# Kernel optimization log

Measured on AMD Instinct MI355X. Metric: run time of the kernel, lower is better.

The kernel has to match this reference:

```python
import jax, jax.numpy as jnp
import numpy as np

B, T, D, H = 4, 2048, 1024, 16
DEPTH = D // H
MASK_NEG = 1e10


def setup_inputs() -> dict:
    key = jax.random.key(0)
    k1, k2, k3 = jax.random.split(key, 3)
    x = jax.random.normal(k1, (B, T, D), dtype=jnp.float32)
    w_attn = jax.random.normal(k2, (D, 3 * D), dtype=jnp.float32) * 0.02
    b_attn = jnp.zeros((3 * D,), dtype=jnp.float32)
    w_proj = jax.random.normal(k3, (D, D), dtype=jnp.float32) * 0.02
    b_proj = jnp.zeros((D,), dtype=jnp.float32)
    return {"x": x, "w_attn": w_attn, "b_attn": b_attn,
            "w_proj": w_proj, "b_proj": b_proj}


def _split_heads(t):
    # (B, T, D) -> (B, H, T, depth)
    return t.reshape(B, T, H, DEPTH).transpose(0, 2, 1, 3)


def reference(x, w_attn, b_attn, w_proj, b_proj):
    # fused QKV projection (GPT-2 conv1d == dense)
    qkv = x @ w_attn + b_attn                      # (B, T, 3D)
    q, k, v = jnp.split(qkv, 3, axis=2)
    q, k, v = _split_heads(q), _split_heads(k), _split_heads(v)
    present = jnp.stack([k, v], axis=1)            # (B, 2, H, T, depth)

    # scaled scores with additive causal mask (as in source: w*b - 1e10*(1-b))
    scores = jnp.einsum('bhqd,bhkd->bhqk', q, k) / jnp.sqrt(
        jnp.asarray(DEPTH, dtype=x.dtype))
    i = jnp.arange(T)[:, None]
    j = jnp.arange(T)[None, :]
    b = (i >= j).astype(scores.dtype)              # (T, T) lower-tri incl diag
    scores = scores * b - MASK_NEG * (1.0 - b)
    attn = jax.nn.softmax(scores, axis=-1)         # (B, H, T, T)

    out = jnp.einsum('bhqk,bhkd->bhqd', attn, v)   # (B, H, T, depth)
    out = out.transpose(0, 2, 1, 3).reshape(B, T, D)
    out = out @ w_proj + b_proj                    # (B, T, D)
    return out, present
```

## Files before the change

### kernel.cpp

```cpp
#include <hip/hip_runtime.h>
#include <hip/hip_bf16.h>
#include <cstdint>
#include <cstddef>

typedef __bf16 y8 __attribute__((ext_vector_type(8)));
typedef float f4 __attribute__((ext_vector_type(4)));
typedef unsigned short u16t;

#define NB 4
#define TT 2048
#define DD 1024
#define HH 16

static constexpr size_t OUT0 = (size_t)NB * TT * DD;
#define QSCALE 0.180336880111120426f

__device__ __forceinline__ u16t bf16r(float f) {
    union { float f; unsigned u; } x; x.f = f;
    return (u16t)((x.u + 0x7FFFu + ((x.u >> 16) & 1u)) >> 16);
}

__device__ __forceinline__ unsigned cvtpk(float lo, float hi) {
    unsigned r;
    asm("v_cvt_pk_bf16_f32 %0, %1, %2" : "=v"(r) : "v"(lo), "v"(hi));
    return r;
}

#define GLDS16(g, s) __builtin_amdgcn_global_load_lds( \
    (__attribute__((address_space(1))) void*)(g),      \
    (__attribute__((address_space(3))) void*)(s), 16, 0, 0)

#define BARX() asm volatile("s_barrier" ::: "memory")
#define VMW(n) asm volatile("s_waitcnt vmcnt(" #n ")" ::: "memory")
#define LGKM0() asm volatile("s_waitcnt lgkmcnt(0)" ::: "memory")

__global__ __launch_bounds__(256)
void cvt_f32_bf16(const float* __restrict__ in, u16t* __restrict__ outp, int n) {
    int i = (blockIdx.x * 256 + threadIdx.x) * 8;
    if (i >= n) return;
    float4 a = *(const float4*)(in + i);
    float4 b = *(const float4*)(in + i + 4);
    union { u16t h[8]; uint4 q; } u;
    u.h[0] = bf16r(a.x); u.h[1] = bf16r(a.y); u.h[2] = bf16r(a.z); u.h[3] = bf16r(a.w);
    u.h[4] = bf16r(b.x); u.h[5] = bf16r(b.y); u.h[6] = bf16r(b.z); u.h[7] = bf16r(b.w);
    *(uint4*)(outp + i) = u.q;
}

__global__ __launch_bounds__(256)
void transpose_w(const float* __restrict__ in, u16t* __restrict__ outp, int Kd, int Nd,
                 int qlim, float qs) {
    __shared__ float tile[32][33];
    const int n0 = blockIdx.x * 32, k0 = blockIdx.y * 32;
    const int tx = threadIdx.x & 31, ty = threadIdx.x >> 5;
    for (int yy = ty; yy < 32; yy += 8)
        tile[yy][tx] = in[(size_t)(k0 + yy) * Nd + n0 + tx];
    __syncthreads();
    for (int yy = ty; yy < 32; yy += 8) {
        float v = tile[tx][yy];
        if (n0 + yy < qlim) v *= qs;
        outp[(size_t)(n0 + yy) * Kd + k0 + tx] = bf16r(v);
    }
}

template<int MODE>
__global__ __launch_bounds__(512, 1)
void gemm_bt(const u16t* __restrict__ A, const u16t* __restrict__ Bt,
             const float* __restrict__ bias, float* __restrict__ C,
             float* __restrict__ pres, u16t* __restrict__ qb,
             u16t* __restrict__ kb, u16t* __restrict__ vtb,
             int N, int K)
{
    __shared__ char sm[98304];
    char* const smA0 = sm;
    char* const smB0 = sm + 65536;
    const int tid = threadIdx.x;
    const int w = tid >> 6, l = tid & 63;
    const int wr = w >> 1, wc = w & 1;
    const int lr = l & 15, lq = l >> 4;
    const int idx = blockIdx.x;
    const int bm = (idx & 31) << 8;
    const int bn = (idx >> 5) << 7;

    auto stage = [&](int k0, int pi) {
#pragma unroll
        for (int c = 0; c < 4; ++c) {
            const int L = (tid << 4) + (c << 13);
            const int row = L >> 7;
            const int col = (((L >> 4) & 7) ^ (row & 7)) << 3;
            GLDS16(A + (size_t)(bm + row) * K + k0 + col,
                   smA0 + (pi << 15) + L);
        }
#pragma unroll
        for (int c = 0; c < 2; ++c) {
            const int L = (tid << 4) + (c << 13);
            const int row = L >> 7;
            const int col = (((L >> 4) & 7) ^ (row & 7)) << 3;
            GLDS16(Bt + (size_t)(bn + row) * K + k0 + col,
                   smB0 + (pi << 14) + L);
        }
    };

    f4 acc[4][4] = {};
    const int nt = K >> 6;

    stage(0, 0);
    for (int t = 0; t < nt; ++t) {
        if (t + 1 < nt) { stage((t + 1) << 6, (t + 1) & 1); VMW(6); }
        else            { VMW(0); }
        BARX();
        const char* La = smA0 + ((t & 1) << 15);
        const char* Lb = smB0 + ((t & 1) << 14);
#pragma unroll
        for (int ks = 0; ks < 2; ++ks) {
            y8 af[4], bfv[4];
#pragma unroll
            for (int m = 0; m < 4; ++m) {
                const int row = wr * 64 + m * 16 + lr;
                const int slot = (lq + ks * 4) ^ (row & 7);
                af[m] = *(const y8*)(La + row * 128 + (slot << 4));
            }
#pragma unroll
            for (int n = 0; n < 4; ++n) {
                const int row = wc * 64 + n * 16 + lr;
                const int slot = (lq + ks * 4) ^ (row & 7);
                bfv[n] = *(const y8*)(Lb + row * 128 + (slot << 4));
            }
#pragma unroll
            for (int m = 0; m < 4; ++m)
#pragma unroll
                for (int n = 0; n < 4; ++n)
                    acc[m][n] = __builtin_amdgcn_mfma_f32_16x16x32_bf16(af[m], bfv[n], acc[m][n], 0, 0, 0);
        }
        BARX();
    }

    if (MODE == 0) {
#pragma unroll
        for (int m = 0; m < 4; ++m) {
            const int rowb = bm + wr * 64 + m * 16 + 4 * lq;
#pragma unroll
            for (int n = 0; n < 4; ++n) {
                const int col = bn + wc * 64 + n * 16 + lr;
                const float bv = bias[col];
#pragma unroll
                for (int r = 0; r < 4; ++r)
                    C[(size_t)(rowb + r) * N + col] = acc[m][n][r] + bv;
            }
        }
    } else {
        const int part = bn >> 10;

        if (part == 2) {
#pragma unroll
            for (int m = 0; m < 4; ++m) {
                const int rowb = bm + wr * 64 + m * 16 + 4 * lq;
                const int b0 = rowb >> 11, t0 = rowb & 2047;
#pragma unroll
                for (int n = 0; n < 4; ++n) {
                    const int colg = bn + wc * 64 + n * 16 + lr;
                    const float bv = bias[colg];
                    const int cl = colg & 1023;
                    const int h = cl >> 6, d = cl & 63;
                    uint2 pk;
                    pk.x = cvtpk(acc[m][n][0] + bv, acc[m][n][1] + bv);
                    pk.y = cvtpk(acc[m][n][2] + bv, acc[m][n][3] + bv);
                    *(uint2*)(vtb + ((size_t)(b0 * HH + h) * 64 + d) * TT + t0) = pk;
                }
            }
        }

#pragma unroll
        for (int m = 0; m < 4; ++m)
#pragma unroll
            for (int n = 0; n < 4; ++n) {
                const int co = wc * 64 + n * 16 + lr;
                float bv = bias[bn + co];
                if (part == 0) bv *= QSCALE;
#pragma unroll
                for (int r = 0; r < 4; ++r) {
                    const int ro = wr * 64 + m * 16 + 4 * lq + r;
                    *(u16t*)(smA0 + ro * 256 + (((co >> 3) ^ (ro & 7)) << 4)
                             + ((co & 7) << 1)) = bf16r(acc[m][n][r] + bv);
                }
            }
        LGKM0();
        BARX();

        const int hb = (bn & 1023) >> 6;
        const int c = tid & 15;
        const int rw = tid >> 4;
        const int h2 = hb + (c >> 3);
        const int d0 = (c & 7) * 8;
#pragma unroll
        for (int s = 0; s < 8; ++s) {
            const int row = s * 32 + rw;
            union { y8 v; uint4 q; u16t h[8]; } u;
            u.v = *(const y8*)(smA0 + row * 256 + ((c ^ (row & 7)) << 4));
            const int tglob = bm + row;
            const int b0 = tglob >> 11, tt = tglob & 2047;
            const size_t base = (((size_t)(b0 * HH + h2)) * TT + tt) * 64 + d0;
            if (part == 0) {
                *(uint4*)(qb + base) = u.q;
            } else {
                if (part == 1) *(uint4*)(kb + base) = u.q;
                float4 f0, f1;
                f0.x = __uint_as_float((unsigned)u.h[0] << 16);
                f0.y = __uint_as_float((unsigned)u.h[1] << 16);
                f0.z = __uint_as_float((unsigned)u.h[2] << 16);
                f0.w = __uint_as_float((unsigned)u.h[3] << 16);
                f1.x = __uint_as_float((unsigned)u.h[4] << 16);
                f1.y = __uint_as_float((unsigned)u.h[5] << 16);
                f1.z = __uint_as_float((unsigned)u.h[6] << 16);
                f1.w = __uint_as_float((unsigned)u.h[7] << 16);
                const size_t pb = OUT0 +
                    (((size_t)((b0 * 2 + (part - 1)) * HH + h2)) * TT + tt) * 64 + d0;
                *(float4*)(pres + pb) = f0;
                *(float4*)(pres + pb + 4) = f1;
            }
        }
    }
}

__global__ __launch_bounds__(256, 3)
void attn_fwd(const u16t* __restrict__ qg, const u16t* __restrict__ kg,
              const u16t* __restrict__ vtg, u16t* __restrict__ og)
{
    __shared__ u16t sQP[128 * 64];
    __shared__ u16t sK[2 * 64 * 64];
    __shared__ u16t sV[2 * 64 * 64];
    const int tid = threadIdx.x;
    const int w = tid >> 6, l = tid & 63;
    const int lr = l & 15, lq = l >> 4;
    const int qt = 15 - blockIdx.y;
    const int bh = blockIdx.x;
    const int b = bh >> 4, h = bh & 15;
    const u16t* qsrc = qg + (size_t)bh * TT * 64;
    const u16t* ksrc = kg + (size_t)bh * TT * 64;
    const u16t* vsrc = vtg + (size_t)bh * 64 * TT;

    auto stageKV = [&](int kt, int pi) {
        const int kv0 = kt << 6;
#pragma unroll
        for (int c = 0; c < 2; ++c) {
            const int L = ((w * 64 + l) << 4) + (c << 12);
            const int row = L >> 7;
            const int col = (((L >> 4) & 7) ^ (row & 7)) << 3;
            GLDS16(ksrc + (kv0 + row) * 64 + col,
                   (char*)sK + (pi << 13) + (w << 10) + (c << 12));
            GLDS16(vsrc + (size_t)row * TT + kv0 + col,
                   (char*)sV + (pi << 13) + (w << 10) + (c << 12));
        }
    };

#pragma unroll
    for (int c = 0; c < 4; ++c) {
        const int L = ((w * 64 + l) << 4) + (c << 12);
        const int row = L >> 7;
        const int col = (((L >> 4) & 7) ^ (row & 7)) << 3;
        GLDS16(qsrc + (qt * 128 + row) * 64 + col, (char*)sQP + (w << 10) + (c << 12));
    }
    stageKV(0, 0);
    __syncthreads();

    y8 qf[2][2];
#pragma unroll
    for (int qm = 0; qm < 2; ++qm)
#pragma unroll
        for (int ks = 0; ks < 2; ++ks) {
            const int row = w * 32 + qm * 16 + lr;
            const int slot = (lq + ks * 4) ^ (row & 7);
            qf[qm][ks] = *(const y8*)((const char*)sQP + row * 128 + (slot << 4));
        }

    f4 o[2][4] = {};
    float lsum[2] = {0.f, 0.f};

    char* Pw = (char*)sQP + (w << 12);
    const int qmax = qt * 128 + w * 32 + 31;
    const int ktiles = 2 * qt + 2;
    int cur = 0;

    for (int kt = 0; kt < ktiles; ++kt) {
        __syncthreads();
        if (kt + 1 < ktiles) stageKV(kt + 1, cur ^ 1);
        const int kv0 = kt << 6;
        if (kv0 <= qmax) {
            const char* Kb = (const char*)sK + (cur << 13);
            const char* Vb = (const char*)sV + (cur << 13);

            f4 s[2][4] = {};
            __builtin_amdgcn_s_setprio(1);
#pragma unroll
            for (int ks = 0; ks < 2; ++ks) {
                y8 kf[4];
#pragma unroll
                for (int n = 0; n < 4; ++n) {
                    const int row = n * 16 + lr;
                    const int slot = (lq + ks * 4) ^ (row & 7);
                    kf[n] = *(const y8*)(Kb + row * 128 + (slot << 4));
                }
#pragma unroll
                for (int qm = 0; qm < 2; ++qm)
#pragma unroll
                    for (int n = 0; n < 4; ++n)
                        s[qm][n] = __builtin_amdgcn_mfma_f32_16x16x32_bf16(kf[n], qf[qm][ks], s[qm][n], 0, 0, 0);
            }
            __builtin_amdgcn_s_setprio(0);

#pragma unroll
            for (int qm = 0; qm < 2; ++qm) {
                const int qb0 = qt * 128 + w * 32 + qm * 16;
                if (kv0 + 63 > qb0) {
                    const int query = qb0 + lr;
#pragma unroll
                    for (int n = 0; n < 4; ++n)
#pragma unroll
                        for (int r = 0; r < 4; ++r)
                            if (kv0 + n * 16 + 4 * lq + r > query) s[qm][n][r] = -1e30f;
                }

                float rs = 0.f;
#pragma unroll
                for (int n = 0; n < 4; ++n)
#pragma unroll
                    for (int r = 0; r < 4; ++r) {
                        const float p = exp2f(s[qm][n][r]);
                        s[qm][n][r] = p;
                        rs += p;
                    }
                lsum[qm] += rs;

                const int prow = qm * 16 + lr;
                const int rbase = prow * 128 + ((lq & 1) << 3);
#pragma unroll
                for (int n = 0; n < 4; ++n) {
                    uint2 pk;
                    pk.x = cvtpk(s[qm][n][0], s[qm][n][1]);
                    pk.y = cvtpk(s[qm][n][2], s[qm][n][3]);
                    const int sIdx = 2 * n + (lq >> 1);
                    *(uint2*)(Pw + rbase + ((sIdx ^ (prow & 7)) << 4)) = pk;
                }
            }

            __builtin_amdgcn_s_setprio(1);
#pragma unroll
            for (int ks = 0; ks < 2; ++ks) {
                y8 vf[4], pf[2];
#pragma unroll
                for (int n = 0; n < 4; ++n) {
                    const int row = n * 16 + lr;
                    const int slot = (lq + ks * 4) ^ (row & 7);
                    vf[n] = *(const y8*)(Vb + row * 128 + (slot << 4));
                }
#pragma unroll
                for (int qm = 0; qm < 2; ++qm) {
                    const int row = qm * 16 + lr;
                    const int slot = (lq + ks * 4) ^ (row & 7);
                    pf[qm] = *(const y8*)(Pw + row * 128 + (slot << 4));
                }
#pragma unroll
                for (int qm = 0; qm < 2; ++qm)
#pragma unroll
                    for (int n = 0; n < 4; ++n)
                        o[qm][n] = __builtin_amdgcn_mfma_f32_16x16x32_bf16(vf[n], pf[qm], o[qm][n], 0, 0, 0);
            }
            __builtin_amdgcn_s_setprio(0);
        }
        cur ^= 1;
    }

#pragma unroll
    for (int qm = 0; qm < 2; ++qm) {
        float t = lsum[qm];
        t += __shfl_xor(t, 16);
        t += __shfl_xor(t, 32);
        const float inv = 1.0f / t;
        const int trow = qt * 128 + w * 32 + qm * 16 + lr;
#pragma unroll
        for (int n = 0; n < 4; ++n) {
            uint2 pk;
            pk.x = cvtpk(o[qm][n][0] * inv, o[qm][n][1] * inv);
            pk.y = cvtpk(o[qm][n][2] * inv, o[qm][n][3] * inv);
            *(uint2*)(og + ((size_t)(b * TT + trow)) * DD + h * 64 + n * 16 + 4 * lq) = pk;
        }
    }
}

extern "C" void kernel_launch(void* const* d_in, const int* in_sizes, int n_in,
                              void* d_out, int out_size, void* d_ws, size_t ws_size,
                              hipStream_t stream) {
    const float* x      = (const float*)d_in[0];
    const float* w_attn = (const float*)d_in[1];
    const float* b_attn = (const float*)d_in[2];
    const float* w_proj = (const float*)d_in[3];
    const float* b_proj = (const float*)d_in[4];
    float* outp = (float*)d_out;
    char* ws = (char*)d_ws;

    u16t* xb  = (u16t*)(ws + 0);
    u16t* wta = (u16t*)(ws + 16777216);
    u16t* wtp = (u16t*)(ws + 23068672);
    u16t* qb  = (u16t*)(ws + 25165824);
    u16t* kb  = (u16t*)(ws + 41943040);
    u16t* vtb = (u16t*)(ws + 58720256);
    if (ws_size < 75497472) return;

    cvt_f32_bf16<<<4096, 256, 0, stream>>>(x, xb, 8388608);
    transpose_w<<<dim3(96, 32), 256, 0, stream>>>(w_attn, wta, 1024, 3072, 1024, QSCALE);
    transpose_w<<<dim3(32, 32), 256, 0, stream>>>(w_proj, wtp, 1024, 1024, 0, 1.0f);

    gemm_bt<1><<<768, 512, 0, stream>>>(xb, wta, b_attn, nullptr, outp,
                                        qb, kb, vtb, 3072, 1024);
    attn_fwd<<<dim3(64, 16), 256, 0, stream>>>(qb, kb, vtb, xb );
    gemm_bt<0><<<256, 512, 0, stream>>>(xb, wtp, b_proj, outp,
                                        nullptr, nullptr, nullptr, nullptr,
                                        1024, 1024);
}
```

Before: 179.0 us.

## Fuse prep kernels into one launch and double attention query tile to 256

Merges the three preprocessing kernels (x conversion and two weight transposes) into one launch with a block-index switch, removing two launch gaps. The attention kernel now uses 512 threads (8 waves) per block, covering 256 query rows instead of 128. Each staged K/V tile is therefore reused by twice as many waves, halving K/V traffic per query. The trade-off is half as many blocks (512), coarser causal load balance, and more LDS per block.

```diff
diff --git a/kernel.cpp b/kernel.cpp
--- a/kernel.cpp
+++ b/kernel.cpp
@@ -35,22 +35,32 @@
 #define LGKM0() asm volatile("s_waitcnt lgkmcnt(0)" ::: "memory")
 
 __global__ __launch_bounds__(256)
-void cvt_f32_bf16(const float* __restrict__ in, u16t* __restrict__ outp, int n) {
-    int i = (blockIdx.x * 256 + threadIdx.x) * 8;
-    if (i >= n) return;
-    float4 a = *(const float4*)(in + i);
-    float4 b = *(const float4*)(in + i + 4);
-    union { u16t h[8]; uint4 q; } u;
-    u.h[0] = bf16r(a.x); u.h[1] = bf16r(a.y); u.h[2] = bf16r(a.z); u.h[3] = bf16r(a.w);
-    u.h[4] = bf16r(b.x); u.h[5] = bf16r(b.y); u.h[6] = bf16r(b.z); u.h[7] = bf16r(b.w);
-    *(uint4*)(outp + i) = u.q;
-}
-
-__global__ __launch_bounds__(256)
-void transpose_w(const float* __restrict__ in, u16t* __restrict__ outp, int Kd, int Nd,
-                 int qlim, float qs) {
+void prep(const float* __restrict__ x, u16t* __restrict__ xb,
+          const float* __restrict__ w_attn, u16t* __restrict__ wta,
+          const float* __restrict__ w_proj, u16t* __restrict__ wtp)
+{
+    const int bid = blockIdx.x;
+    if (bid < 4096) {
+        const int i = (bid * 256 + threadIdx.x) * 8;
+        float4 a = *(const float4*)(x + i);
+        float4 b = *(const float4*)(x + i + 4);
+        union { u16t h[8]; uint4 q; } u;
+        u.h[0] = bf16r(a.x); u.h[1] = bf16r(a.y); u.h[2] = bf16r(a.z); u.h[3] = bf16r(a.w);
+        u.h[4] = bf16r(b.x); u.h[5] = bf16r(b.y); u.h[6] = bf16r(b.z); u.h[7] = bf16r(b.w);
+        *(uint4*)(xb + i) = u.q;
+        return;
+    }
     __shared__ float tile[32][33];
-    const int n0 = blockIdx.x * 32, k0 = blockIdx.y * 32;
+    const float* in; u16t* outp; int Nd, n0, k0, qlim; float qs;
+    if (bid < 7168) {
+        const int j = bid - 4096;
+        in = w_attn; outp = wta; Nd = 3072;
+        n0 = (j % 96) * 32; k0 = (j / 96) * 32; qlim = 1024; qs = QSCALE;
+    } else {
+        const int j = bid - 7168;
+        in = w_proj; outp = wtp; Nd = 1024;
+        n0 = (j & 31) * 32; k0 = (j >> 5) * 32; qlim = 0; qs = 1.0f;
+    }
     const int tx = threadIdx.x & 31, ty = threadIdx.x >> 5;
     for (int yy = ty; yy < 32; yy += 8)
         tile[yy][tx] = in[(size_t)(k0 + yy) * Nd + n0 + tx];
@@ -58,7 +68,7 @@
     for (int yy = ty; yy < 32; yy += 8) {
         float v = tile[tx][yy];
         if (n0 + yy < qlim) v *= qs;
-        outp[(size_t)(n0 + yy) * Kd + k0 + tx] = bf16r(v);
+        outp[(size_t)(n0 + yy) * 1024 + k0 + tx] = bf16r(v);
     }
 }
 
@@ -221,17 +231,17 @@
     }
 }
 
-__global__ __launch_bounds__(256, 3)
+__global__ __launch_bounds__(512, 4)
 void attn_fwd(const u16t* __restrict__ qg, const u16t* __restrict__ kg,
               const u16t* __restrict__ vtg, u16t* __restrict__ og)
 {
-    __shared__ u16t sQP[128 * 64];
+    __shared__ u16t sQP[256 * 64];
     __shared__ u16t sK[2 * 64 * 64];
     __shared__ u16t sV[2 * 64 * 64];
     const int tid = threadIdx.x;
     const int w = tid >> 6, l = tid & 63;
     const int lr = l & 15, lq = l >> 4;
-    const int qt = 15 - blockIdx.y;
+    const int qt = 7 - blockIdx.y;
     const int bh = blockIdx.x;
     const int b = bh >> 4, h = bh & 15;
     const u16t* qsrc = qg + (size_t)bh * TT * 64;
@@ -240,24 +250,19 @@
 
     auto stageKV = [&](int kt, int pi) {
         const int kv0 = kt << 6;
-#pragma unroll
-        for (int c = 0; c < 2; ++c) {
-            const int L = ((w * 64 + l) << 4) + (c << 12);
-            const int row = L >> 7;
-            const int col = (((L >> 4) & 7) ^ (row & 7)) << 3;
-            GLDS16(ksrc + (kv0 + row) * 64 + col,
-                   (char*)sK + (pi << 13) + (w << 10) + (c << 12));
-            GLDS16(vsrc + (size_t)row * TT + kv0 + col,
-                   (char*)sV + (pi << 13) + (w << 10) + (c << 12));
-        }
-    };
-
-#pragma unroll
-    for (int c = 0; c < 4; ++c) {
-        const int L = ((w * 64 + l) << 4) + (c << 12);
+        const int L = tid << 4;
         const int row = L >> 7;
         const int col = (((L >> 4) & 7) ^ (row & 7)) << 3;
-        GLDS16(qsrc + (qt * 128 + row) * 64 + col, (char*)sQP + (w << 10) + (c << 12));
+        GLDS16(ksrc + (kv0 + row) * 64 + col, (char*)sK + (pi << 13) + L);
+        GLDS16(vsrc + (size_t)row * TT + kv0 + col, (char*)sV + (pi << 13) + L);
+    };
+
+#pragma unroll
+    for (int c = 0; c < 4; ++c) {
+        const int L = (tid << 4) + (c << 13);
+        const int row = L >> 7;
+        const int col = (((L >> 4) & 7) ^ (row & 7)) << 3;
+        GLDS16(qsrc + (qt * 256 + row) * 64 + col, (char*)sQP + L);
     }
     stageKV(0, 0);
     __syncthreads();
@@ -276,8 +281,8 @@
     float lsum[2] = {0.f, 0.f};
 
     char* Pw = (char*)sQP + (w << 12);
-    const int qmax = qt * 128 + w * 32 + 31;
-    const int ktiles = 2 * qt + 2;
+    const int qmax = qt * 256 + w * 32 + 31;
+    const int ktiles = 4 * qt + 4;
     int cur = 0;
 
     for (int kt = 0; kt < ktiles; ++kt) {
@@ -309,7 +314,7 @@
 
 #pragma unroll
             for (int qm = 0; qm < 2; ++qm) {
-                const int qb0 = qt * 128 + w * 32 + qm * 16;
+                const int qb0 = qt * 256 + w * 32 + qm * 16;
                 if (kv0 + 63 > qb0) {
                     const int query = qb0 + lr;
 #pragma unroll
@@ -375,7 +380,7 @@
         t += __shfl_xor(t, 16);
         t += __shfl_xor(t, 32);
         const float inv = 1.0f / t;
-        const int trow = qt * 128 + w * 32 + qm * 16 + lr;
+        const int trow = qt * 256 + w * 32 + qm * 16 + lr;
 #pragma unroll
         for (int n = 0; n < 4; ++n) {
             uint2 pk;
@@ -405,13 +410,11 @@
     u16t* vtb = (u16t*)(ws + 58720256);
     if (ws_size < 75497472) return;
 
-    cvt_f32_bf16<<<4096, 256, 0, stream>>>(x, xb, 8388608);
-    transpose_w<<<dim3(96, 32), 256, 0, stream>>>(w_attn, wta, 1024, 3072, 1024, QSCALE);
-    transpose_w<<<dim3(32, 32), 256, 0, stream>>>(w_proj, wtp, 1024, 1024, 0, 1.0f);
+    prep<<<8192, 256, 0, stream>>>(x, xb, w_attn, wta, w_proj, wtp);
 
     gemm_bt<1><<<768, 512, 0, stream>>>(xb, wta, b_attn, nullptr, outp,
                                         qb, kb, vtb, 3072, 1024);
-    attn_fwd<<<dim3(64, 16), 256, 0, stream>>>(qb, kb, vtb, xb );
+    attn_fwd<<<dim3(64, 8), 512, 0, stream>>>(qb, kb, vtb, xb );
     gemm_bt<0><<<256, 512, 0, stream>>>(xb, wtp, b_proj, outp,
                                         nullptr, nullptr, nullptr, nullptr,
                                         1024, 1024);
```

Result: slower. 198.9 us (+11.1%).
